# Kernel tuning notes

Hardware: AMD Instinct MI355X
Metric: run time of the kernel (lower is better)

The kernel has to match this reference:

```python
import jax, jax.numpy as jnp
import numpy as np

B, L, D_IN = 16, 2048, 512
HID, H = 512, 8
D = HID // H          # head dim
FACTOR = 5
U = min(FACTOR * int(np.ceil(np.log(L))), L)  # u_q == u_k == 40 (L == S)


def setup_inputs() -> dict:
    key = jax.random.key(0)
    ks = jax.random.split(key, 8)
    s = 1.0 / np.sqrt(D_IN).astype(np.float32)
    return {
        "q_in": jax.random.normal(ks[0], (B, L, D_IN), jnp.float32),
        "k_in": jax.random.normal(ks[1], (B, L, D_IN), jnp.float32),
        "v_in": jax.random.normal(ks[2], (B, L, D_IN), jnp.float32),
        "Wq": jax.random.normal(ks[3], (D_IN, HID), jnp.float32) * s,
        "Wk": jax.random.normal(ks[4], (D_IN, HID), jnp.float32) * s,
        "Wv": jax.random.normal(ks[5], (D_IN, HID), jnp.float32) * s,
        "Wo": jax.random.normal(ks[6], (HID, HID // H), jnp.float32) / np.sqrt(HID).astype(np.float32),
        "indx_q_seq": jax.random.randint(ks[7], (L,), 0, L, dtype=jnp.int32),
    }


def reference(q_in, k_in, v_in, Wq, Wk, Wv, Wo, indx_q_seq):
    # projections + (memory-reinterpreting, as in the TF source) head reshape
    q = (q_in @ Wq).reshape(B, H, L, D)
    k = (k_in @ Wk).reshape(B, H, L, D)
    v = (v_in @ Wv).reshape(B, H, L, D)

    # --- _prob_qk ---
    # TF's chained gathers on the broadcast k_expand collapse to pairing
    # query s with the single key indx_q_seq[s]; all sample_k columns of
    # Q_K_sample are identical, so M = max - sum/L = dot * (1 - U/L).
    k_sel = k[:, :, indx_q_seq, :]                        # [B,H,L,D]
    dot = jnp.einsum('bhle,bhle->bhl', q, k_sel)          # [B,H,L]
    M = dot - dot * (jnp.float32(U) / jnp.float32(L))
    _, m_top = jax.lax.top_k(M, U)                        # [B,H,U]

    b_idx = jnp.arange(B)[:, None, None]
    h_idx = jnp.arange(H)[None, :, None]
    q_red = q[b_idx, h_idx, m_top]                        # [B,H,U,D]
    scores = jnp.einsum('bhue,bhle->bhul', q_red, k)      # [B,H,U,L]
    scores = scores * (1.0 / np.sqrt(D).astype(np.float32))

    # --- initial context: causal cumsum of values ---
    context = jnp.cumsum(v, axis=-2)                      # [B,H,L,D]

    # --- update context at the top-U query positions (causal mask) ---
    causal = jnp.arange(L)[None, None, None, :] > m_top[..., None]
    scores = jnp.where(causal, -jnp.inf, scores)
    attn = jax.nn.softmax(scores, axis=-1)                # [B,H,U,L]
    upd = jnp.einsum('bhul,bhld->bhud', attn, v)          # [B,H,U,D]
    context = context.at[b_idx, h_idx, m_top].set(upd)

    out = context.reshape(B, L, HID) @ Wo                 # [B,L,HID//H]
    return out
```

## Files before the change

kernel.cpp:

```cpp
#include <hip/hip_runtime.h>
#include <hip/hip_bf16.h>
#include <math.h>

#define B_   16
#define L_   2048
#define DIN  512
#define HID_ 512
#define H_   8
#define D_   64
#define U_   40
#define BH   (B_*H_)

typedef unsigned short u16;
typedef unsigned int u32;
typedef unsigned long long u64;
typedef __bf16 bf16x8 __attribute__((ext_vector_type(8)));
typedef float f32x4 __attribute__((ext_vector_type(4)));

__device__ __forceinline__ u16 f2bf(float x) {
  __bf16 b = (__bf16)x;
  return __builtin_bit_cast(unsigned short, b);
}
__device__ __forceinline__ float bf2f(u16 h) {
  return __uint_as_float(((unsigned)h) << 16);
}
__device__ __forceinline__ u32 pk2(float a, float b) {
  return (u32)f2bf(a) | ((u32)f2bf(b) << 16);
}
__device__ __forceinline__ void gload16(const u16* g, u16* l) {
  __builtin_amdgcn_global_load_lds(
      (__attribute__((address_space(1))) void*)(g),
      (__attribute__((address_space(3))) void*)(l), 16, 0, 0);
}
__device__ __forceinline__ void gload16f(const float* g, float* l) {
  __builtin_amdgcn_global_load_lds(
      (__attribute__((address_space(1))) void*)(g),
      (__attribute__((address_space(3))) void*)(l), 16, 0, 0);
}
__device__ __forceinline__ u64 mkkey(float Mv, int l) {
  u32 fb = __float_as_uint(Mv);
  u32 mapped = (fb & 0x80000000u) ? ~fb : (fb | 0x80000000u);
  return ((u64)mapped << 32) | (u64)(0xFFFFFFFFu - (u32)l);
}

__global__ __launch_bounds__(256)
void wsplit3_kernel(const float* __restrict__ Wq, const float* __restrict__ Wk,
                    const float* __restrict__ Wv, u16* __restrict__ Bt3) {
  const float* W = (blockIdx.y == 0) ? Wq : (blockIdx.y == 1) ? Wk : Wv;
  u16* Bt = Bt3 + (size_t)blockIdx.y * 524288;
  int tid = blockIdx.x * 256 + threadIdx.x;
  int n = tid & 511, k = tid >> 9;
  float a = W[(size_t)k * 512 + n];
  u16 hi = f2bf(a);
  u16 lo = f2bf(a - bf2f(hi));
  int kb = k >> 5, kc = k & 31;
  int slotH = kc >> 3, wi = kc & 7;
  int swzH = (slotH     ^ (n & 7)) << 3;
  int swzL = ((4+slotH) ^ (n & 7)) << 3;
  Bt[(size_t)n * 1024 + kb * 64 + swzH + wi] = hi;
  Bt[(size_t)n * 1024 + kb * 64 + swzL + wi] = lo;
}

__global__ __launch_bounds__(256, 2)
void gemm_proj3(const float* __restrict__ A, const u16* __restrict__ Bt,
                float* __restrict__ C) {
  __shared__ float Asf[2][128 * 32];
  __shared__ u16 Bs[2][128 * 64];
  const int bid = blockIdx.x;
  const int g = bid >> 3;
  const int xb = (bid & 7) + ((g >> 2) << 3);
  const int yb = g & 3;
  const int t = threadIdx.x;
  const int w = t >> 6, lane = t & 63;
  const int lhi = lane >> 4, l16 = lane & 15;
  const int row0 = xb * 128, col0 = yb * 128;
  const int wrow = (w >> 1) * 64, wcol = (w & 1) * 64;

  const u16* gB = Bt + (size_t)(col0 + w * 32 + (lane >> 3)) * 1024 + (lane & 7) * 8;
  const int rA0 = w * 32 + (lane >> 3);
  const int swsl = lane & 7;

  f32x4 acc[4][4];
  #pragma unroll
  for (int i = 0; i < 4; ++i)
    #pragma unroll
    for (int j = 0; j < 4; ++j) acc[i][j] = (f32x4){0.f, 0.f, 0.f, 0.f};

#define STAGE3(KB, NB)                                                          \
  { u16* lB = &Bs[NB][(w * 32) * 64];                                           \
    _Pragma("unroll") for (int i = 0; i < 4; ++i)                               \
      gload16(gB + (KB) * 64 + (size_t)i * 8 * 1024, lB + i * 8 * 64);          \
    _Pragma("unroll") for (int i = 0; i < 4; ++i) {                             \
      int r = rA0 + i * 8;                                                      \
      int slot = swsl ^ (r & 7);                                                \
      gload16f(A + (size_t)(row0 + r) * 512 + (KB) * 32 + slot * 4,             \
               &Asf[NB][(w * 32 + i * 8) * 32]); } }

  STAGE3(0, 0)
  __syncthreads();

  for (int kb = 0; kb < 16; ++kb) {
    const int cur = kb & 1;
    if (kb < 15) STAGE3(kb + 1, cur ^ 1)

    bf16x8 bfH[4], bfL[4];
    #pragma unroll
    for (int j = 0; j < 4; ++j) {
      int cb = wcol + j * 16 + l16;
      bfH[j] = *reinterpret_cast<const bf16x8*>(
          &Bs[cur][cb * 64 + ((lhi ^ (cb & 7)) << 3)]);
      bfL[j] = *reinterpret_cast<const bf16x8*>(
          &Bs[cur][cb * 64 + (((4 + lhi) ^ (cb & 7)) << 3)]);
    }
    #pragma unroll
    for (int i = 0; i < 4; ++i) {
      int ra = wrow + i * 16 + l16;
      const f32x4 x0 = *reinterpret_cast<const f32x4*>(
          &Asf[cur][ra * 32 + (((lhi * 2)       ^ (ra & 7)) << 2)]);
      const f32x4 x1 = *reinterpret_cast<const f32x4*>(
          &Asf[cur][ra * 32 + ((((lhi * 2) + 1) ^ (ra & 7)) << 2)]);
      bf16x8 aH;
      aH[0] = (__bf16)x0[0]; aH[1] = (__bf16)x0[1];
      aH[2] = (__bf16)x0[2]; aH[3] = (__bf16)x0[3];
      aH[4] = (__bf16)x1[0]; aH[5] = (__bf16)x1[1];
      aH[6] = (__bf16)x1[2]; aH[7] = (__bf16)x1[3];
      #pragma unroll
      for (int j = 0; j < 4; ++j)
        acc[i][j] = __builtin_amdgcn_mfma_f32_16x16x32_bf16(aH, bfH[j], acc[i][j], 0, 0, 0);
      bf16x8 aL;
      aL[0] = (__bf16)(x0[0] - (float)aH[0]); aL[1] = (__bf16)(x0[1] - (float)aH[1]);
      aL[2] = (__bf16)(x0[2] - (float)aH[2]); aL[3] = (__bf16)(x0[3] - (float)aH[3]);
      aL[4] = (__bf16)(x1[0] - (float)aH[4]); aL[5] = (__bf16)(x1[1] - (float)aH[5]);
      aL[6] = (__bf16)(x1[2] - (float)aH[6]); aL[7] = (__bf16)(x1[3] - (float)aH[7]);
      #pragma unroll
      for (int j = 0; j < 4; ++j)
        acc[i][j] = __builtin_amdgcn_mfma_f32_16x16x32_bf16(aH, bfL[j], acc[i][j], 0, 0, 0);
      #pragma unroll
      for (int j = 0; j < 4; ++j)
        acc[i][j] = __builtin_amdgcn_mfma_f32_16x16x32_bf16(aL, bfH[j], acc[i][j], 0, 0, 0);
    }
    __syncthreads();
  }
#undef STAGE3
  #pragma unroll
  for (int i = 0; i < 4; ++i)
    #pragma unroll
    for (int j = 0; j < 4; ++j)
      #pragma unroll
      for (int r = 0; r < 4; ++r)
        C[(size_t)(row0 + wrow + i * 16 + lhi * 4 + r) * 512
          + col0 + wcol + j * 16 + l16] = acc[i][j][r];
}

__global__ __launch_bounds__(256, 2)
void gemm_proj_v(const float* __restrict__ A, const u16* __restrict__ Bt,
                 u16* __restrict__ C) {
  __shared__ float Asf[2][128 * 32];
  __shared__ u16 Bs[2][128 * 64];
  const int bid = blockIdx.x;
  const int g = bid >> 3;
  const int xb = (bid & 7) + ((g >> 2) << 3);
  const int yb = g & 3;
  const int t = threadIdx.x;
  const int w = t >> 6, lane = t & 63;
  const int lhi = lane >> 4, l16 = lane & 15;
  const int row0 = xb * 128, col0 = yb * 128;
  const int wrow = (w >> 1) * 64, wcol = (w & 1) * 64;

  const u16* gB = Bt + (size_t)(col0 + w * 32 + (lane >> 3)) * 1024 + (lane & 7) * 8;
  const int rA0 = w * 32 + (lane >> 3);
  const int swsl = lane & 7;

  f32x4 acc[4][4];
  #pragma unroll
  for (int i = 0; i < 4; ++i)
    #pragma unroll
    for (int j = 0; j < 4; ++j) acc[i][j] = (f32x4){0.f, 0.f, 0.f, 0.f};

#define STAGEV(KB, NB)                                                          \
  { u16* lB = &Bs[NB][(w * 32) * 64];                                           \
    _Pragma("unroll") for (int i = 0; i < 4; ++i)                               \
      gload16(gB + (KB) * 64 + (size_t)i * 8 * 1024, lB + i * 8 * 64);          \
    _Pragma("unroll") for (int i = 0; i < 4; ++i) {                             \
      int r = rA0 + i * 8;                                                      \
      int slot = swsl ^ (r & 7);                                                \
      gload16f(A + (size_t)(row0 + r) * 512 + (KB) * 32 + slot * 4,             \
               &Asf[NB][(w * 32 + i * 8) * 32]); } }

  STAGEV(0, 0)
  __syncthreads();

  for (int kb = 0; kb < 16; ++kb) {
    const int cur = kb & 1;
    if (kb < 15) STAGEV(kb + 1, cur ^ 1)
    bf16x8 bfH[4];
    #pragma unroll
    for (int j = 0; j < 4; ++j) {
      int cb = wcol + j * 16 + l16;
      bfH[j] = *reinterpret_cast<const bf16x8*>(
          &Bs[cur][cb * 64 + ((lhi ^ (cb & 7)) << 3)]);
    }
    #pragma unroll
    for (int i = 0; i < 4; ++i) {
      int ra = wrow + i * 16 + l16;
      const f32x4 x0 = *reinterpret_cast<const f32x4*>(
          &Asf[cur][ra * 32 + (((lhi * 2)       ^ (ra & 7)) << 2)]);
      const f32x4 x1 = *reinterpret_cast<const f32x4*>(
          &Asf[cur][ra * 32 + ((((lhi * 2) + 1) ^ (ra & 7)) << 2)]);
      bf16x8 aH;
      aH[0] = (__bf16)x0[0]; aH[1] = (__bf16)x0[1];
      aH[2] = (__bf16)x0[2]; aH[3] = (__bf16)x0[3];
      aH[4] = (__bf16)x1[0]; aH[5] = (__bf16)x1[1];
      aH[6] = (__bf16)x1[2]; aH[7] = (__bf16)x1[3];
      #pragma unroll
      for (int j = 0; j < 4; ++j)
        acc[i][j] = __builtin_amdgcn_mfma_f32_16x16x32_bf16(aH, bfH[j], acc[i][j], 0, 0, 0);
    }
    __syncthreads();
  }
#undef STAGEV
  #pragma unroll
  for (int i = 0; i < 4; ++i)
    #pragma unroll
    for (int j = 0; j < 4; ++j)
      #pragma unroll
      for (int r = 0; r < 4; ++r)
        C[(size_t)(row0 + wrow + i * 16 + lhi * 4 + r) * 512
          + col0 + wcol + j * 16 + l16] = f2bf(acc[i][j][r]);
}

__global__ __launch_bounds__(256)
void dotsel_kernel(const float* __restrict__ qp, const float* __restrict__ kp,
                   const int* __restrict__ indx, u64* __restrict__ cand) {
  __shared__ u64 keys[256];
  __shared__ u64 wl[192];
  const int bh = blockIdx.x, ch = blockIdx.y;
  const int t = threadIdx.x, w = t >> 6, lane = t & 63;
  const size_t boff = (size_t)bh * 131072;
  const int l0 = ch * 256 + w * 64;
  const float cUL = 40.0f / 2048.0f;
  const int li = lane >> 4;
  const int dq = lane & 15;

  if (t >= 160 && t < 192) wl[t] = 0;

  #pragma unroll 4
  for (int i = 0; i < 16; ++i) {
    int l = l0 + i * 4 + li;
    int ls = indx[l];
    float4 q4 = *reinterpret_cast<const float4*>(&qp[boff + (size_t)l * 64 + dq * 4]);
    float4 k4 = *reinterpret_cast<const float4*>(&kp[boff + (size_t)ls * 64 + dq * 4]);
    float p = q4.x * k4.x + q4.y * k4.y + q4.z * k4.z + q4.w * k4.w;
    p += __shfl_xor(p, 1, 64);
    p += __shfl_xor(p, 2, 64);
    p += __shfl_xor(p, 4, 64);
    p += __shfl_xor(p, 8, 64);
    if (dq == 0) {
      float Mv = p - p * cUL;
      keys[w * 64 + i * 4 + li] = mkkey(Mv, l);
    }
  }
  __syncthreads();

  u64 myk = keys[t];
  for (int u = 0; u < U_; ++u) {
    u64 b = myk;
    #pragma unroll
    for (int off = 32; off >= 1; off >>= 1) {
      u64 v = __shfl_xor(b, off, 64);
      if (v > b) b = v;
    }
    if (myk == b) myk = 0;
    if (lane == 0) wl[w * 40 + u] = b;
  }
  __syncthreads();

  if (w == 0) {
    u64 c0 = wl[lane], c1 = wl[64 + lane], c2 = wl[128 + lane];
    for (int u = 0; u < U_; ++u) {
      u64 b = c0;
      if (c1 > b) b = c1;
      if (c2 > b) b = c2;
      #pragma unroll
      for (int off = 32; off >= 1; off >>= 1) {
        u64 v = __shfl_xor(b, off, 64);
        if (v > b) b = v;
      }
      if (c0 == b) c0 = 0;
      if (c1 == b) c1 = 0;
      if (c2 == b) c2 = 0;
      if (lane == 0) cand[((size_t)(bh * 8 + ch)) * U_ + u] = b;
    }
  }
}

__global__ __launch_bounds__(64)
void merge_topk(const u64* __restrict__ cand, int* __restrict__ mtop) {
  const int bh = blockIdx.x;
  const int lane = threadIdx.x;
  u64 c0 = cand[(size_t)bh * 320 + 0 * 64 + lane];
  u64 c1 = cand[(size_t)bh * 320 + 1 * 64 + lane];
  u64 c2 = cand[(size_t)bh * 320 + 2 * 64 + lane];
  u64 c3 = cand[(size_t)bh * 320 + 3 * 64 + lane];
  u64 c4 = cand[(size_t)bh * 320 + 4 * 64 + lane];
  for (int u = 0; u < U_; ++u) {
    u64 b = c0;
    if (c1 > b) b = c1;
    if (c2 > b) b = c2;
    if (c3 > b) b = c3;
    if (c4 > b) b = c4;
    #pragma unroll
    for (int off = 32; off >= 1; off >>= 1) {
      u64 v = __shfl_xor(b, off, 64);
      if (v > b) b = v;
    }
    if (c0 == b) c0 = 0;
    if (c1 == b) c1 = 0;
    if (c2 == b) c2 = 0;
    if (c3 == b) c3 = 0;
    if (c4 == b) c4 = 0;
    if (lane == 0) mtop[bh * U_ + u] = (int)(0xFFFFFFFFu - (u32)b);
  }
}

__global__ __launch_bounds__(256)
void gather_q_kernel(const float* __restrict__ qp, const int* __restrict__ mtop,
                     u16* __restrict__ qredbf) {
  int tid = blockIdx.x * 256 + threadIdx.x;
  int s = tid >> 6;
  int d = tid & 63;
  int bh = s / 48;
  int u = s - bh * 48;
  float val = 0.f;
  if (u < U_) {
    int m = mtop[bh * U_ + u];
    val = qp[(size_t)bh * (L_ * D_) + (size_t)m * D_ + d] * 0.125f;
  }
  qredbf[tid] = f2bf(val);
}

__global__ __launch_bounds__(256)
void attn_fused(const u16* __restrict__ qredbf, const float* __restrict__ kp,
                const u16* __restrict__ vbf, const int* __restrict__ mtop,
                float* __restrict__ partial, float* __restrict__ msums) {
  __shared__ u16 As[48 * 64];
  __shared__ u16 Bs[128 * 64];
  __shared__ u16 Ps[48 * 128];
  __shared__ int ms[48];
  __shared__ float redm[4][48];
  __shared__ float reds[4][48];
  const int bh = blockIdx.x, chk = blockIdx.y;
  const int l0 = chk * 128;
  const int t = threadIdx.x, w = t >> 6, lane = t & 63;
  const int lhi = lane >> 4, l16 = lane & 15;

  for (int e = t; e < 384; e += 256) {
    int r = e >> 3, s = e & 7;
    *reinterpret_cast<uint4*>(&As[r * 64 + ((s ^ (r & 7)) << 3)]) =
        *reinterpret_cast<const uint4*>(&qredbf[(size_t)bh * 3072 + e * 8]);
  }
  #pragma unroll
  for (int ee = 0; ee < 4; ++ee) {
    int e = t + ee * 256;
    int r = e >> 3, s = e & 7;
    const float* src = &kp[(size_t)bh * 131072 + (size_t)(l0 + r) * 64 + s * 8];
    float4 va = *reinterpret_cast<const float4*>(src);
    float4 vb = *reinterpret_cast<const float4*>(src + 4);
    uint4 w4 = make_uint4(pk2(va.x, va.y), pk2(va.z, va.w),
                          pk2(vb.x, vb.y), pk2(vb.z, vb.w));
    *reinterpret_cast<uint4*>(&Bs[r * 64 + ((s ^ (r & 7)) << 3)]) = w4;
  }
  if (t < 48) ms[t] = (t < U_) ? mtop[bh * U_ + t] : -1;
  __syncthreads();

  f32x4 acc[3][2];
  #pragma unroll
  for (int m = 0; m < 3; ++m)
    #pragma unroll
    for (int n = 0; n < 2; ++n) acc[m][n] = (f32x4){0.f, 0.f, 0.f, 0.f};
  #pragma unroll
  for (int ks = 0; ks < 2; ++ks) {
    bf16x8 a[3], b[2];
    #pragma unroll
    for (int m = 0; m < 3; ++m) {
      int r = m * 16 + l16;
      a[m] = *reinterpret_cast<const bf16x8*>(
          &As[r * 64 + (((ks * 4 + lhi) ^ (r & 7)) << 3)]);
    }
    #pragma unroll
    for (int n = 0; n < 2; ++n) {
      int cb = w * 32 + n * 16 + l16;
      b[n] = *reinterpret_cast<const bf16x8*>(
          &Bs[cb * 64 + (((ks * 4 + lhi) ^ (cb & 7)) << 3)]);
    }
    #pragma unroll
    for (int m = 0; m < 3; ++m)
      #pragma unroll
      for (int n = 0; n < 2; ++n)
        acc[m][n] = __builtin_amdgcn_mfma_f32_16x16x32_bf16(a[m], b[n], acc[m][n], 0, 0, 0);
  }

  float val[3][2][4], mx[3][4];
  #pragma unroll
  for (int m = 0; m < 3; ++m)
    #pragma unroll
    for (int r = 0; r < 4; ++r) {
      int u = m * 16 + lhi * 4 + r;
      float v0 = acc[m][0][r], v1 = acc[m][1][r];
      if (l0 + w * 32 + 0 * 16 + l16 > ms[u]) v0 = -INFINITY;
      if (l0 + w * 32 + 1 * 16 + l16 > ms[u]) v1 = -INFINITY;
      val[m][0][r] = v0; val[m][1][r] = v1;
      mx[m][r] = fmaxf(v0, v1);
    }
  #pragma unroll
  for (int off = 1; off <= 8; off <<= 1)
    #pragma unroll
    for (int m = 0; m < 3; ++m)
      #pragma unroll
      for (int r = 0; r < 4; ++r)
        mx[m][r] = fmaxf(mx[m][r], __shfl_xor(mx[m][r], off, 64));
  if (l16 == 0) {
    #pragma unroll
    for (int m = 0; m < 3; ++m)
      #pragma unroll
      for (int r = 0; r < 4; ++r)
        redm[w][m * 16 + lhi * 4 + r] = mx[m][r];
  }
  __syncthreads();

  float sx[3][4];
  #pragma unroll
  for (int m = 0; m < 3; ++m)
    #pragma unroll
    for (int r = 0; r < 4; ++r) {
      int u = m * 16 + lhi * 4 + r;
      float mv = fmaxf(fmaxf(redm[0][u], redm[1][u]), fmaxf(redm[2][u], redm[3][u]));
      mv = (mv > -1e30f) ? mv : 0.f;
      float p0 = __expf(val[m][0][r] - mv);
      float p1 = __expf(val[m][1][r] - mv);
      sx[m][r] = p0 + p1;
      {
        int l = w * 32 + 0 * 16 + l16, s = l >> 3;
        int sw = (s & 8) | ((s & 7) ^ (u & 7));
        Ps[u * 128 + (sw << 3) + (l & 7)] = f2bf(p0);
      }
      {
        int l = w * 32 + 1 * 16 + l16, s = l >> 3;
        int sw = (s & 8) | ((s & 7) ^ (u & 7));
        Ps[u * 128 + (sw << 3) + (l & 7)] = f2bf(p1);
      }
    }
  #pragma unroll
  for (int off = 1; off <= 8; off <<= 1)
    #pragma unroll
    for (int m = 0; m < 3; ++m)
      #pragma unroll
      for (int r = 0; r < 4; ++r)
        sx[m][r] += __shfl_xor(sx[m][r], off, 64);
  if (l16 == 0) {
    #pragma unroll
    for (int m = 0; m < 3; ++m)
      #pragma unroll
      for (int r = 0; r < 4; ++r)
        reds[w][m * 16 + lhi * 4 + r] = sx[m][r];
  }
  __syncthreads();

  if (t < 48) {
    float mv = fmaxf(fmaxf(redm[0][t], redm[1][t]), fmaxf(redm[2][t], redm[3][t]));
    mv = (mv > -1e30f) ? mv : 0.f;
    float sv = reds[0][t] + reds[1][t] + reds[2][t] + reds[3][t];
    size_t o = (((size_t)chk * 128 + bh) * 48 + t) * 2;
    msums[o] = mv; msums[o + 1] = sv;
  }
  const size_t vbase = (size_t)bh * 131072;
  #pragma unroll
  for (int j = 0; j < 16; ++j) {
    int ll = w * 32 + 2 * j;
    u16 ua = vbf[vbase + (size_t)(l0 + ll) * 64 + lane];
    u16 ub = vbf[vbase + (size_t)(l0 + ll + 1) * 64 + lane];
    u32 pk = (u32)ua | ((u32)ub << 16);
    int s = ll >> 3;
    int sw = (s & 8) | ((s & 7) ^ (lane & 7));
    *reinterpret_cast<u32*>(&Bs[lane * 128 + (sw << 3) + (ll & 7)]) = pk;
  }
  __syncthreads();

  f32x4 acc2[3];
  #pragma unroll
  for (int m = 0; m < 3; ++m) acc2[m] = (f32x4){0.f, 0.f, 0.f, 0.f};
  #pragma unroll
  for (int ks = 0; ks < 4; ++ks) {
    bf16x8 b;
    { int cb = w * 16 + l16; int s = ks * 4 + lhi;
      int sw = (s & 8) | ((s & 7) ^ (cb & 7));
      b = *reinterpret_cast<const bf16x8*>(&Bs[cb * 128 + (sw << 3)]); }
    #pragma unroll
    for (int m = 0; m < 3; ++m) {
      int r = m * 16 + l16; int s = ks * 4 + lhi;
      int sw = (s & 8) | ((s & 7) ^ (r & 7));
      bf16x8 a = *reinterpret_cast<const bf16x8*>(&Ps[r * 128 + (sw << 3)]);
      acc2[m] = __builtin_amdgcn_mfma_f32_16x16x32_bf16(a, b, acc2[m], 0, 0, 0);
    }
  }
  #pragma unroll
  for (int m = 0; m < 3; ++m)
    #pragma unroll
    for (int r = 0; r < 4; ++r) {
      int u = m * 16 + lhi * 4 + r;
      partial[(((size_t)chk * 128 + bh) * 48 + u) * 64 + w * 16 + l16] = acc2[m][r];
    }
}

__global__ __launch_bounds__(256)
void merge_pv(const float* __restrict__ partial, const float* __restrict__ msums,
              float* __restrict__ upd) {
  int tid = blockIdx.x * 256 + threadIdx.x;
  int s = tid >> 6, d = tid & 63;
  int bh = s / U_, u = s - bh * U_;
  float mg = -INFINITY;
  #pragma unroll
  for (int c = 0; c < 16; ++c)
    mg = fmaxf(mg, msums[(((size_t)c * 128 + bh) * 48 + u) * 2]);
  float av = 0.f, sg = 0.f;
  #pragma unroll
  for (int c = 0; c < 16; ++c) {
    size_t o = (((size_t)c * 128 + bh) * 48 + u) * 2;
    float e = __expf(msums[o] - mg);
    av += partial[(((size_t)c * 128 + bh) * 48 + u) * 64 + d] * e;
    sg += msums[o + 1] * e;
  }
  upd[(size_t)s * 64 + d] = av / sg;
}

__global__ __launch_bounds__(256)
void cumsumA(const u16* __restrict__ vbf, float* __restrict__ seg32) {
  int bh = blockIdx.x, sg = blockIdx.y;
  int t = threadIdx.x, w = t >> 6, lane = t & 63;
  int g = sg * 4 + w;
  size_t base = (size_t)bh * 131072 + (size_t)g * 32 * 64;
  float s = 0.f;
  for (int i = 0; i < 32; ++i) s += bf2f(vbf[base + i * 64 + lane]);
  seg32[((size_t)bh * 64 + g) * 64 + lane] = s;
}
__global__ __launch_bounds__(256)
void cumsumB(const u16* __restrict__ vbf, const float* __restrict__ seg32,
             u16* __restrict__ ctxbf) {
  int bh = blockIdx.x, sg = blockIdx.y;
  int t = threadIdx.x, w = t >> 6, lane = t & 63;
  int g = sg * 4 + w;
  float run = 0.f;
  for (int s = 0; s < g; ++s) run += seg32[((size_t)bh * 64 + s) * 64 + lane];
  size_t base = (size_t)bh * 131072 + (size_t)g * 32 * 64;
  for (int i = 0; i < 32; ++i) {
    run += bf2f(vbf[base + i * 64 + lane]);
    ctxbf[base + i * 64 + lane] = f2bf(run);
  }
}

__global__ __launch_bounds__(256)
void scatter_kernel(const float* __restrict__ upd, const int* __restrict__ mtop,
                    u16* __restrict__ ctxbf) {
  int tid = blockIdx.x * 256 + threadIdx.x;
  int s = tid >> 6;
  if (s >= BH * U_) return;
  int d = tid & 63;
  int bh = s / U_;
  ctxbf[(size_t)bh * 131072 + (size_t)mtop[s] * 64 + d] = f2bf(upd[(size_t)s * 64 + d]);
}

__global__ __launch_bounds__(256)
void wo_prep(const float* __restrict__ Wo, u16* __restrict__ WoT) {
  int tid = blockIdx.x * 256 + threadIdx.x;
  int j = tid >> 9, k = tid & 511;
  float v = Wo[(size_t)k * 64 + j];
  int k0 = k & ~63, ko = k & 63;
  int ks = ko >> 5, kc = ko & 31;
  int slot = (ks * 4 + (kc >> 3)) ^ (j & 7);
  WoT[(size_t)j * 512 + k0 + (slot << 3) + (kc & 7)] = f2bf(v);
}

__global__ __launch_bounds__(256, 6)
void gemm_out(const u16* __restrict__ ctxbf, const u16* __restrict__ WoT,
              float* __restrict__ out) {
  __shared__ u16 As[64 * 64];
  __shared__ u16 Bs[64 * 64];
  const int t = threadIdx.x, w = t >> 6, lane = t & 63;
  const int lhi = lane >> 4, l16 = lane & 15;
  const int row0 = blockIdx.x * 64;
  f32x4 acc[4];
  #pragma unroll
  for (int j = 0; j < 4; ++j) acc[j] = (f32x4){0.f, 0.f, 0.f, 0.f};

  for (int k0 = 0; k0 < 512; k0 += 64) {
    #pragma unroll
    for (int ii = 0; ii < 2; ++ii) {
      int e = t + ii * 256;
      int j = e >> 3, s = e & 7;
      gload16(WoT + (size_t)j * 512 + k0 + s * 8, Bs + (size_t)(w * 64 + ii * 256) * 8);
    }
    #pragma unroll
    for (int ii = 0; ii < 2; ++ii) {
      int e = t + ii * 256;
      int r = e >> 3, s = e & 7;
      gload16(ctxbf + (size_t)(row0 + r) * 512 + k0 + (s ^ (r & 7)) * 8,
              As + (size_t)(w * 64 + ii * 256) * 8);
    }
    __syncthreads();
    #pragma unroll
    for (int ks = 0; ks < 2; ++ks) {
      int r = w * 16 + l16;
      bf16x8 a = *reinterpret_cast<const bf16x8*>(
          &As[r * 64 + (((ks * 4 + lhi) ^ (r & 7)) << 3)]);
      #pragma unroll
      for (int jf = 0; jf < 4; ++jf) {
        int cb = jf * 16 + l16;
        bf16x8 b = *reinterpret_cast<const bf16x8*>(
            &Bs[cb * 64 + (((ks * 4 + lhi) ^ (cb & 7)) << 3)]);
        acc[jf] = __builtin_amdgcn_mfma_f32_16x16x32_bf16(a, b, acc[jf], 0, 0, 0);
      }
    }
    __syncthreads();
  }
  #pragma unroll
  for (int jf = 0; jf < 4; ++jf)
    #pragma unroll
    for (int r = 0; r < 4; ++r)
      out[(size_t)(row0 + w * 16 + lhi * 4 + r) * 64 + jf * 16 + l16] = acc[jf][r];
}

extern "C" void kernel_launch(void* const* d_in, const int* in_sizes, int n_in,
                              void* d_out, int out_size, void* d_ws, size_t ws_size,
                              hipStream_t stream) {
  const float* q_in = (const float*)d_in[0];
  const float* k_in = (const float*)d_in[1];
  const float* v_in = (const float*)d_in[2];
  const float* Wq   = (const float*)d_in[3];
  const float* Wk   = (const float*)d_in[4];
  const float* Wv   = (const float*)d_in[5];
  const float* Wo   = (const float*)d_in[6];
  const int*   indx = (const int*)d_in[7];
  float* out = (float*)d_out;

  float* ws = (float*)d_ws;
  float* qp   = ws;
  float* kp   = ws + 16777216;
  u16*   vbf  = (u16*)(ws + 33554432);
  u64*   cand = (u64*)(ws + 50331648);
  u16*   WoT  = (u16*)cand;
  u16*   qredbf = (u16*)(ws + 50593792);
  int*   mtop = (int*)(ws + 50921472);
  u16*   Bt3  = (u16*)d_out;
  float* partial = qp;
  float* msums   = qp + 6291456;
  float* upd     = qp + 6488064;
  u16*   ctxbf = (u16*)kp;
  float* seg32 = kp + 8388608;

  const int M = B_ * L_;

  wsplit3_kernel<<<dim3(1024, 3), 256, 0, stream>>>(Wq, Wk, Wv, Bt3);

  gemm_proj3<<<1024, 256, 0, stream>>>(q_in, Bt3, qp);
  gemm_proj3<<<1024, 256, 0, stream>>>(k_in, Bt3 + 524288, kp);
  gemm_proj_v<<<1024, 256, 0, stream>>>(v_in, Bt3 + 1048576, vbf);

  dotsel_kernel<<<dim3(BH, 8), 256, 0, stream>>>(qp, kp, indx, cand);
  merge_topk<<<BH, 64, 0, stream>>>(cand, mtop);
  gather_q_kernel<<<(BH * 48 * 64) / 256, 256, 0, stream>>>(qp, mtop, qredbf);

  attn_fused<<<dim3(BH, 16), 256, 0, stream>>>(qredbf, kp, vbf, mtop, partial, msums);
  merge_pv<<<(BH * U_ * 64) / 256, 256, 0, stream>>>(partial, msums, upd);

  cumsumA<<<dim3(BH, 16), 256, 0, stream>>>(vbf, seg32);
  cumsumB<<<dim3(BH, 16), 256, 0, stream>>>(vbf, seg32, ctxbf);

  scatter_kernel<<<(BH * U_ * 64) / 256, 256, 0, stream>>>(upd, mtop, ctxbf);

  wo_prep<<<128, 256, 0, stream>>>(Wo, WoT);
  gemm_out<<<M / 64, 256, 0, stream>>>(ctxbf, WoT, out);
}
```

Measured before the change: 375.6 us.

## Refine GEMM barriers, restructure block top-k, fuse merge/scatter and Wo prep

The projection GEMMs replace __syncthreads with explicit vmcnt waits plus raw s_barrier and sched_barrier, so the prefetch of the next stage can stay in flight while the current one is consumed. The dotsel top-k now reduces across all four waves each round through a small shared max array, which removes the second wave-0 merge pass. merge_pv and scatter are fused into one kernel, and the Wo transpose/prep is folded into merge_topk, cutting three launches and the upd round-trip. WoT moves to its own workspace slot so it no longer aliases cand. The hand-placed waits depend on exact load counts per stage and could break if the compiler reorders or splits loads.

```diff
diff --git a/kernel.cpp b/kernel.cpp
--- a/kernel.cpp
+++ b/kernel.cpp
@@ -97,11 +97,19 @@
                &Asf[NB][(w * 32 + i * 8) * 32]); } }
 
   STAGE3(0, 0)
-  __syncthreads();
+  asm volatile("s_waitcnt vmcnt(0)" ::: "memory");
+  __builtin_amdgcn_s_barrier();
 
   for (int kb = 0; kb < 16; ++kb) {
     const int cur = kb & 1;
-    if (kb < 15) STAGE3(kb + 1, cur ^ 1)
+    if (kb < 15) {
+      STAGE3(kb + 1, cur ^ 1)
+      asm volatile("s_waitcnt vmcnt(8)" ::: "memory");
+    } else {
+      asm volatile("s_waitcnt vmcnt(0)" ::: "memory");
+    }
+    __builtin_amdgcn_sched_barrier(0);
+    __builtin_amdgcn_s_barrier();
 
     bf16x8 bfH[4], bfL[4];
     #pragma unroll
@@ -139,7 +147,8 @@
       for (int j = 0; j < 4; ++j)
         acc[i][j] = __builtin_amdgcn_mfma_f32_16x16x32_bf16(aL, bfH[j], acc[i][j], 0, 0, 0);
     }
-    __syncthreads();
+    __builtin_amdgcn_s_barrier();
+    __builtin_amdgcn_sched_barrier(0);
   }
 #undef STAGE3
   #pragma unroll
@@ -188,11 +197,20 @@
                &Asf[NB][(w * 32 + i * 8) * 32]); } }
 
   STAGEV(0, 0)
-  __syncthreads();
+  asm volatile("s_waitcnt vmcnt(0)" ::: "memory");
+  __builtin_amdgcn_s_barrier();
 
   for (int kb = 0; kb < 16; ++kb) {
     const int cur = kb & 1;
-    if (kb < 15) STAGEV(kb + 1, cur ^ 1)
+    if (kb < 15) {
+      STAGEV(kb + 1, cur ^ 1)
+      asm volatile("s_waitcnt vmcnt(8)" ::: "memory");
+    } else {
+      asm volatile("s_waitcnt vmcnt(0)" ::: "memory");
+    }
+    __builtin_amdgcn_sched_barrier(0);
+    __builtin_amdgcn_s_barrier();
+
     bf16x8 bfH[4];
     #pragma unroll
     for (int j = 0; j < 4; ++j) {
@@ -216,7 +234,8 @@
       for (int j = 0; j < 4; ++j)
         acc[i][j] = __builtin_amdgcn_mfma_f32_16x16x32_bf16(aH, bfH[j], acc[i][j], 0, 0, 0);
     }
-    __syncthreads();
+    __builtin_amdgcn_s_barrier();
+    __builtin_amdgcn_sched_barrier(0);
   }
 #undef STAGEV
   #pragma unroll
@@ -233,7 +252,7 @@
 void dotsel_kernel(const float* __restrict__ qp, const float* __restrict__ kp,
                    const int* __restrict__ indx, u64* __restrict__ cand) {
   __shared__ u64 keys[256];
-  __shared__ u64 wl[192];
+  __shared__ u64 wmax[2][4];
   const int bh = blockIdx.x, ch = blockIdx.y;
   const int t = threadIdx.x, w = t >> 6, lane = t & 63;
   const size_t boff = (size_t)bh * 131072;
@@ -242,9 +261,7 @@
   const int li = lane >> 4;
   const int dq = lane & 15;
 
-  if (t >= 160 && t < 192) wl[t] = 0;
-
-  #pragma unroll 4
+  #pragma unroll 8
   for (int i = 0; i < 16; ++i) {
     int l = l0 + i * 4 + li;
     int ls = indx[l];
@@ -270,34 +287,34 @@
       u64 v = __shfl_xor(b, off, 64);
       if (v > b) b = v;
     }
-    if (myk == b) myk = 0;
-    if (lane == 0) wl[w * 40 + u] = b;
-  }
-  __syncthreads();
-
-  if (w == 0) {
-    u64 c0 = wl[lane], c1 = wl[64 + lane], c2 = wl[128 + lane];
-    for (int u = 0; u < U_; ++u) {
-      u64 b = c0;
-      if (c1 > b) b = c1;
-      if (c2 > b) b = c2;
-      #pragma unroll
-      for (int off = 32; off >= 1; off >>= 1) {
-        u64 v = __shfl_xor(b, off, 64);
-        if (v > b) b = v;
-      }
-      if (c0 == b) c0 = 0;
-      if (c1 == b) c1 = 0;
-      if (c2 == b) c2 = 0;
-      if (lane == 0) cand[((size_t)(bh * 8 + ch)) * U_ + u] = b;
-    }
-  }
-}
-
-__global__ __launch_bounds__(64)
-void merge_topk(const u64* __restrict__ cand, int* __restrict__ mtop) {
+    if (lane == 0) wmax[u & 1][w] = b;
+    __syncthreads();
+    const u64* wm = wmax[u & 1];
+    u64 m = wm[0];
+    if (wm[1] > m) m = wm[1];
+    if (wm[2] > m) m = wm[2];
+    if (wm[3] > m) m = wm[3];
+    if (myk == m) myk = 0;
+    if (t == 0) cand[((size_t)(bh * 8 + ch)) * U_ + u] = m;
+  }
+}
+
+__global__ __launch_bounds__(256)
+void merge_topk_wo(const u64* __restrict__ cand, int* __restrict__ mtop,
+                   const float* __restrict__ Wo, u16* __restrict__ WoT) {
   const int bh = blockIdx.x;
-  const int lane = threadIdx.x;
+  const int t = threadIdx.x;
+  {
+    int tid = bh * 256 + t;
+    int j = tid >> 9, k = tid & 511;
+    float v = Wo[(size_t)k * 64 + j];
+    int k0 = k & ~63, ko = k & 63;
+    int ks = ko >> 5, kc = ko & 31;
+    int slot = (ks * 4 + (kc >> 3)) ^ (j & 7);
+    WoT[(size_t)j * 512 + k0 + (slot << 3) + (kc & 7)] = f2bf(v);
+  }
+  if (t >= 64) return;
+  const int lane = t;
   u64 c0 = cand[(size_t)bh * 320 + 0 * 64 + lane];
   u64 c1 = cand[(size_t)bh * 320 + 1 * 64 + lane];
   u64 c2 = cand[(size_t)bh * 320 + 2 * 64 + lane];
@@ -513,27 +530,6 @@
 }
 
 __global__ __launch_bounds__(256)
-void merge_pv(const float* __restrict__ partial, const float* __restrict__ msums,
-              float* __restrict__ upd) {
-  int tid = blockIdx.x * 256 + threadIdx.x;
-  int s = tid >> 6, d = tid & 63;
-  int bh = s / U_, u = s - bh * U_;
-  float mg = -INFINITY;
-  #pragma unroll
-  for (int c = 0; c < 16; ++c)
-    mg = fmaxf(mg, msums[(((size_t)c * 128 + bh) * 48 + u) * 2]);
-  float av = 0.f, sg = 0.f;
-  #pragma unroll
-  for (int c = 0; c < 16; ++c) {
-    size_t o = (((size_t)c * 128 + bh) * 48 + u) * 2;
-    float e = __expf(msums[o] - mg);
-    av += partial[(((size_t)c * 128 + bh) * 48 + u) * 64 + d] * e;
-    sg += msums[o + 1] * e;
-  }
-  upd[(size_t)s * 64 + d] = av / sg;
-}
-
-__global__ __launch_bounds__(256)
 void cumsumA(const u16* __restrict__ vbf, float* __restrict__ seg32) {
   int bh = blockIdx.x, sg = blockIdx.y;
   int t = threadIdx.x, w = t >> 6, lane = t & 63;
@@ -559,25 +555,24 @@
 }
 
 __global__ __launch_bounds__(256)
-void scatter_kernel(const float* __restrict__ upd, const int* __restrict__ mtop,
-                    u16* __restrict__ ctxbf) {
+void merge_pv_scatter(const float* __restrict__ partial, const float* __restrict__ msums,
+                      const int* __restrict__ mtop, u16* __restrict__ ctxbf) {
   int tid = blockIdx.x * 256 + threadIdx.x;
-  int s = tid >> 6;
-  if (s >= BH * U_) return;
-  int d = tid & 63;
-  int bh = s / U_;
-  ctxbf[(size_t)bh * 131072 + (size_t)mtop[s] * 64 + d] = f2bf(upd[(size_t)s * 64 + d]);
-}
-
-__global__ __launch_bounds__(256)
-void wo_prep(const float* __restrict__ Wo, u16* __restrict__ WoT) {
-  int tid = blockIdx.x * 256 + threadIdx.x;
-  int j = tid >> 9, k = tid & 511;
-  float v = Wo[(size_t)k * 64 + j];
-  int k0 = k & ~63, ko = k & 63;
-  int ks = ko >> 5, kc = ko & 31;
-  int slot = (ks * 4 + (kc >> 3)) ^ (j & 7);
-  WoT[(size_t)j * 512 + k0 + (slot << 3) + (kc & 7)] = f2bf(v);
+  int s = tid >> 6, d = tid & 63;
+  int bh = s / U_, u = s - bh * U_;
+  float mg = -INFINITY;
+  #pragma unroll
+  for (int c = 0; c < 16; ++c)
+    mg = fmaxf(mg, msums[(((size_t)c * 128 + bh) * 48 + u) * 2]);
+  float av = 0.f, sg = 0.f;
+  #pragma unroll
+  for (int c = 0; c < 16; ++c) {
+    size_t o = (((size_t)c * 128 + bh) * 48 + u) * 2;
+    float e = __expf(msums[o] - mg);
+    av += partial[(((size_t)c * 128 + bh) * 48 + u) * 64 + d] * e;
+    sg += msums[o + 1] * e;
+  }
+  ctxbf[(size_t)bh * 131072 + (size_t)mtop[s] * 64 + d] = f2bf(av / sg);
 }
 
 __global__ __launch_bounds__(256, 6)
@@ -647,13 +642,12 @@
   float* kp   = ws + 16777216;
   u16*   vbf  = (u16*)(ws + 33554432);
   u64*   cand = (u64*)(ws + 50331648);
-  u16*   WoT  = (u16*)cand;
   u16*   qredbf = (u16*)(ws + 50593792);
+  u16*   WoT  = (u16*)(ws + 50790400);
   int*   mtop = (int*)(ws + 50921472);
   u16*   Bt3  = (u16*)d_out;
   float* partial = qp;
   float* msums   = qp + 6291456;
-  float* upd     = qp + 6488064;
   u16*   ctxbf = (u16*)kp;
   float* seg32 = kp + 8388608;
 
@@ -666,17 +660,14 @@
   gemm_proj_v<<<1024, 256, 0, stream>>>(v_in, Bt3 + 1048576, vbf);
 
   dotsel_kernel<<<dim3(BH, 8), 256, 0, stream>>>(qp, kp, indx, cand);
-  merge_topk<<<BH, 64, 0, stream>>>(cand, mtop);
+  merge_topk_wo<<<BH, 256, 0, stream>>>(cand, mtop, Wo, WoT);
   gather_q_kernel<<<(BH * 48 * 64) / 256, 256, 0, stream>>>(qp, mtop, qredbf);
 
   attn_fused<<<dim3(BH, 16), 256, 0, stream>>>(qredbf, kp, vbf, mtop, partial, msums);
-  merge_pv<<<(BH * U_ * 64) / 256, 256, 0, stream>>>(partial, msums, upd);
 
   cumsumA<<<dim3(BH, 16), 256, 0, stream>>>(vbf, seg32);
   cumsumB<<<dim3(BH, 16), 256, 0, stream>>>(vbf, seg32, ctxbf);
-
-  scatter_kernel<<<(BH * U_ * 64) / 256, 256, 0, stream>>>(upd, mtop, ctxbf);
-
-  wo_prep<<<128, 256, 0, stream>>>(Wo, WoT);
+  merge_pv_scatter<<<(BH * U_ * 64) / 256, 256, 0, stream>>>(partial, msums, mtop, ctxbf);
+
   gemm_out<<<M / 64, 256, 0, stream>>>(ctxbf, WoT, out);
 }
```

Measured after the change: 323.2 us. 1.16x faster.
